# Performance work log

Hardware: AMD Instinct MI355X
Metric: run time of the kernel (lower is better)

The kernel has to match this reference:

```python
import jax, jax.numpy as jnp
import numpy as np

TEMP = 0.07
DIAG_FILL = -10.0


def setup_inputs() -> dict:
    key = jax.random.key(0)
    k1, k2 = jax.random.split(key)
    N, D = 8192, 256
    feat_q = jax.random.normal(k1, (N, D), dtype=jnp.float32)
    feat_k = jax.random.normal(k2, (N, D), dtype=jnp.float32)
    return {"feat_q": feat_q, "feat_k": feat_k}


def reference(feat_q, feat_k):
    # feat_k is detached in the original module
    feat_k = jax.lax.stop_gradient(feat_k)
    N = feat_q.shape[0]

    q_norm = jnp.linalg.norm(feat_q, axis=-1, keepdims=True)  # [N,1]
    k_norm = jnp.linalg.norm(feat_k, axis=-1, keepdims=True)  # [N,1]

    # positive logits: cosine similarity of matching patches -> [N,1]
    l_pos = jnp.sum(feat_q * feat_k, axis=-1, keepdims=True) / (q_norm * k_norm)

    # negative logits: pairwise cosine similarities -> [N,N]
    l_neg = jnp.einsum('nd,md->nm', feat_q, feat_k) / (q_norm * k_norm.T)
    # mask diagonal (self pairs) with -10.0
    diag = jnp.eye(N, dtype=bool)
    l_neg = jnp.where(diag, jnp.float32(DIAG_FILL), l_neg)

    out = jnp.concatenate([l_pos, l_neg], axis=1) / TEMP  # [N, 1+N]
    # cross-entropy with target class 0, reduction='none'
    loss = jax.nn.logsumexp(out, axis=1) - out[:, 0]
    return loss
```

## Files before the change

kernel.cpp:

```cpp
#include <hip/hip_runtime.h>
#include <stdint.h>

#define N_ROWS 8192
#define DIM 256

constexpr float INV_T = 1.0f / 0.07f;
constexpr float M0    = 1.0f / 0.07f;
constexpr float LOG2E = 1.44269504088896f;
constexpr float C1    = INV_T * LOG2E;
constexpr float C0    = -M0 * LOG2E;
constexpr float KSCL  = 127.0f / 0.35f;

typedef int i32x4  __attribute__((ext_vector_type(4)));
typedef int i32x16 __attribute__((ext_vector_type(16)));

__device__ inline float fast_exp2(float x) {
    float r;
    asm("v_exp_f32 %0, %1" : "=v"(r) : "v"(x));
    return r;
}
__device__ inline int pack4(int a, int b, int c, int d) {
    return (a & 0xff) | ((b & 0xff) << 8) | ((c & 0xff) << 16) | (d << 24);
}

__global__ __launch_bounds__(256) void prep_kernel(
    const float* __restrict__ q, const float* __restrict__ k,
    int* __restrict__ qi8, int* __restrict__ ki8,
    float* __restrict__ lposT, float* __restrict__ fqs) {
    const int wid  = threadIdx.x >> 6;
    const int lane = threadIdx.x & 63;
    const int row  = blockIdx.x * 4 + wid;

    const float4 qv = *reinterpret_cast<const float4*>(q + (size_t)row * DIM + lane * 4);
    const float4 kv = *reinterpret_cast<const float4*>(k + (size_t)row * DIM + lane * 4);

    float qq = qv.x*qv.x + qv.y*qv.y + qv.z*qv.z + qv.w*qv.w;
    float kk = kv.x*kv.x + kv.y*kv.y + kv.z*kv.z + kv.w*kv.w;
    float qk = qv.x*kv.x + qv.y*kv.y + qv.z*kv.z + qv.w*kv.w;
    float qm = fmaxf(fmaxf(fabsf(qv.x), fabsf(qv.y)), fmaxf(fabsf(qv.z), fabsf(qv.w)));

    #pragma unroll
    for (int off = 32; off > 0; off >>= 1) {
        qq += __shfl_xor(qq, off, 64);
        kk += __shfl_xor(kk, off, 64);
        qk += __shfl_xor(qk, off, 64);
        qm  = fmaxf(qm, __shfl_xor(qm, off, 64));
    }
    const float iq = 1.0f / sqrtf(qq);
    const float ik = 1.0f / sqrtf(kk);

    const float ksc = ik * KSCL;
    int k0 = __float2int_rn(fminf(fmaxf(kv.x * ksc, -127.f), 127.f));
    int k1 = __float2int_rn(fminf(fmaxf(kv.y * ksc, -127.f), 127.f));
    int k2 = __float2int_rn(fminf(fmaxf(kv.z * ksc, -127.f), 127.f));
    int k3 = __float2int_rn(fminf(fmaxf(kv.w * ksc, -127.f), 127.f));
    ki8[(size_t)row * 64 + lane] = pack4(k0, k1, k2, k3);

    const float qsc = 127.0f / qm;
    int q0 = __float2int_rn(qv.x * qsc);
    int q1 = __float2int_rn(qv.y * qsc);
    int q2 = __float2int_rn(qv.z * qsc);
    int q3 = __float2int_rn(qv.w * qsc);
    qi8[(size_t)row * 64 + lane] = pack4(q0, q1, q2, q3);

    if (lane == 0) {
        lposT[row] = qk * iq * ik * INV_T;
        fqs[row] = C1 * (0.35f / (127.0f * 127.0f)) * qm * iq;
    }
}

__global__ __launch_bounds__(256, 2) void gemm_lse_kernel(
    const uint8_t* __restrict__ qi8, const uint8_t* __restrict__ ki8,
    const float* __restrict__ fqs, float* __restrict__ ps) {
    __shared__ char lds[3 * 16384];

    const int tid  = threadIdx.x;
    const int lane = tid & 63;
    const int wid  = tid >> 6;
    const int l31  = lane & 31;
    const int l5   = lane >> 5;

    const int qtile = blockIdx.x;
    const int strip = blockIdx.y;
    const int qw    = qtile * 256 + wid * 64;
    const int ks0   = strip * 512;

    auto stage = [&](int t) {
        char* dst = lds + (t % 3) * 16384;
        const int kr0 = ks0 + t * 64;
        #pragma unroll
        for (int s = 0; s < 4; ++s) {
            const int n    = wid * 4 + s;
            const int lrow = n * 8 + (lane >> 3);
            const int row  = lrow & 63;
            const int kh   = lrow >> 6;
            const uint8_t* gp = ki8 + (size_t)(kr0 + row) * 256 + kh * 128
                              + (((lane & 7) ^ (lrow & 7)) << 4);
            __builtin_amdgcn_global_load_lds(
                (const __attribute__((address_space(1))) void*)gp,
                (__attribute__((address_space(3))) void*)(dst + n * 1024),
                16, 0, 0);
        }
    };

    i32x4 qf[8][2];
    #pragma unroll
    for (int ks = 0; ks < 8; ++ks)
        #pragma unroll
        for (int cg = 0; cg < 2; ++cg)
            qf[ks][cg] = *reinterpret_cast<const i32x4*>(
                qi8 + (size_t)(qw + cg * 32 + l31) * 256 + ks * 32 + l5 * 16);
    const float f0 = fqs[qw + l31];
    const float f1 = fqs[qw + 32 + l31];

    stage(0);
    stage(1);

    i32x16 acc00 = {}, acc01 = {}, acc10 = {}, acc11 = {};
    float ssum0 = 0.f, ssum1 = 0.f;

    auto lda = [&](const char* src, int rg, i32x4* a) {
        const int row = rg * 32 + l31;
        #pragma unroll
        for (int ks = 0; ks < 8; ++ks) {
            const int o    = ks * 32 + l5 * 16;
            const int lrow = row + ((o >> 7) << 6);
            const int slot = ((o & 127) >> 4) ^ (lrow & 7);
            a[ks] = *reinterpret_cast<const i32x4*>(src + lrow * 128 + (slot << 4));
        }
    };

    auto expfrag = [&](i32x16& A, bool diag, float f, float& ss) {
        float s = 0.f;
        #pragma unroll
        for (int r = 0; r < 16; ++r) {
            float e = fast_exp2(fmaf((float)A[r], f, C0));
            if (diag && (((r & 3) + 8 * (r >> 2) + 4 * l5) == l31)) e = 0.f;
            s += e;
            A[r] = 0;
        }
        ss += s;
    };

    auto epilogue = [&](int t) {
        const int kc0 = ks0 + t * 64;
        expfrag(acc00, kc0 == qw, f0, ssum0);
        expfrag(acc01, false,     f1, ssum1);
        expfrag(acc10, false,     f0, ssum0);
        expfrag(acc11, kc0 == qw, f1, ssum1);
    };

    #pragma unroll
    for (int t = 0; t < 8; ++t) {
        if (t < 7) { asm volatile("s_waitcnt vmcnt(4)" ::: "memory"); }
        else       { asm volatile("s_waitcnt vmcnt(0)" ::: "memory"); }
        __builtin_amdgcn_s_barrier();
        __builtin_amdgcn_sched_barrier(0);
        if (t < 6) stage(t + 2);
        if (t > 0) epilogue(t - 1);

        const char* cur = lds + (t % 3) * 16384;
        i32x4 a0[8], a1[8];
        lda(cur, 0, a0);
        __builtin_amdgcn_s_setprio(1);
        #pragma unroll
        for (int ks = 0; ks < 8; ++ks) {
            acc00 = __builtin_amdgcn_mfma_i32_32x32x32_i8(a0[ks], qf[ks][0], acc00, 0, 0, 0);
            acc01 = __builtin_amdgcn_mfma_i32_32x32x32_i8(a0[ks], qf[ks][1], acc01, 0, 0, 0);
        }
        __builtin_amdgcn_s_setprio(0);
        lda(cur, 1, a1);
        __builtin_amdgcn_s_setprio(1);
        #pragma unroll
        for (int ks = 0; ks < 8; ++ks) {
            acc10 = __builtin_amdgcn_mfma_i32_32x32x32_i8(a1[ks], qf[ks][0], acc10, 0, 0, 0);
            acc11 = __builtin_amdgcn_mfma_i32_32x32x32_i8(a1[ks], qf[ks][1], acc11, 0, 0, 0);
        }
        __builtin_amdgcn_s_setprio(0);
    }
    epilogue(7);

    ssum0 += __shfl_xor(ssum0, 32, 64);
    ssum1 += __shfl_xor(ssum1, 32, 64);
    if (lane < 32) {
        ps[(size_t)(qw + l31) * 16 + strip]      = ssum0;
        ps[(size_t)(qw + 32 + l31) * 16 + strip] = ssum1;
    }
}

__global__ __launch_bounds__(256) void finalize_kernel(
    const float* __restrict__ ps, const float* __restrict__ lposT,
    float* __restrict__ out) {
    const int row = blockIdx.x * 256 + threadIdx.x;
    float S = 0.f;
    #pragma unroll
    for (int c = 0; c < 4; ++c) {
        const float4 p = *reinterpret_cast<const float4*>(ps + (size_t)row * 16 + c * 4);
        S += p.x + p.y + p.z + p.w;
    }
    const float lp = lposT[row];
    S += __expf(lp - M0);
    out[row] = M0 + logf(S) - lp;
}

extern "C" void kernel_launch(void* const* d_in, const int* in_sizes, int n_in,
                              void* d_out, int out_size, void* d_ws, size_t ws_size,
                              hipStream_t stream) {
    const float* q = (const float*)d_in[0];
    const float* k = (const float*)d_in[1];
    float* out = (float*)d_out;

    char* ws = (char*)d_ws;
    int*   qi8 = (int*)(ws);
    int*   ki8 = (int*)(ws + (2u << 20));
    float* lpt = (float*)(ws + (4u << 20));
    float* fqs = (float*)(ws + (4u << 20) + (32u << 10));
    float* ps  = (float*)(ws + (4u << 20) + (64u << 10));

    prep_kernel<<<N_ROWS / 4, 256, 0, stream>>>(q, k, qi8, ki8, lpt, fqs);
    dim3 grid(32, 16);
    gemm_lse_kernel<<<grid, 256, 0, stream>>>((const uint8_t*)qi8, (const uint8_t*)ki8, fqs, ps);
    finalize_kernel<<<N_ROWS / 256, 256, 0, stream>>>(ps, lpt, out);
}
```

Before: 36.91 us.

## Halve K-tile to 32 rows per stage and raise occupancy to 3 blocks

Each pipeline stage in the GEMM+LSE kernel now covers 32 key rows instead of 64, which halves the LDS ring buffer and drops from four to two accumulators per wave. The launch bound rises to 3 blocks per CU, and the main loop runs 16 iterations without unrolling. The aim is to cut register and LDS pressure so more waves can hide latency. The cost is twice as many barriers and waitcnts per strip, and a loop that is no longer unrolled.

```diff
diff --git a/kernel.cpp b/kernel.cpp
--- a/kernel.cpp
+++ b/kernel.cpp
@@ -69,10 +69,10 @@
     }
 }
 
-__global__ __launch_bounds__(256, 2) void gemm_lse_kernel(
+__global__ __launch_bounds__(256, 3) void gemm_lse_kernel(
     const uint8_t* __restrict__ qi8, const uint8_t* __restrict__ ki8,
     const float* __restrict__ fqs, float* __restrict__ ps) {
-    __shared__ char lds[3 * 16384];
+    __shared__ char lds[3 * 8192];
 
     const int tid  = threadIdx.x;
     const int lane = tid & 63;
@@ -86,15 +86,15 @@
     const int ks0   = strip * 512;
 
     auto stage = [&](int t) {
-        char* dst = lds + (t % 3) * 16384;
-        const int kr0 = ks0 + t * 64;
-        #pragma unroll
-        for (int s = 0; s < 4; ++s) {
-            const int n    = wid * 4 + s;
+        char* dst = lds + (t % 3) * 8192;
+        const int kr0 = ks0 + t * 32;
+        #pragma unroll
+        for (int s = 0; s < 2; ++s) {
+            const int n    = wid * 2 + s;
             const int lrow = n * 8 + (lane >> 3);
-            const int row  = lrow & 63;
-            const int kh   = lrow >> 6;
-            const uint8_t* gp = ki8 + (size_t)(kr0 + row) * 256 + kh * 128
+            const int row  = lrow & 31;
+            const int h    = lrow >> 5;
+            const uint8_t* gp = ki8 + (size_t)(kr0 + row) * 256 + h * 128
                               + (((lane & 7) ^ (lrow & 7)) << 4);
             __builtin_amdgcn_global_load_lds(
                 (const __attribute__((address_space(1))) void*)gp,
@@ -116,15 +116,14 @@
     stage(0);
     stage(1);
 
-    i32x16 acc00 = {}, acc01 = {}, acc10 = {}, acc11 = {};
+    i32x16 acc0 = {}, acc1 = {};
     float ssum0 = 0.f, ssum1 = 0.f;
 
-    auto lda = [&](const char* src, int rg, i32x4* a) {
-        const int row = rg * 32 + l31;
+    auto lda = [&](const char* src, i32x4* a) {
         #pragma unroll
         for (int ks = 0; ks < 8; ++ks) {
             const int o    = ks * 32 + l5 * 16;
-            const int lrow = row + ((o >> 7) << 6);
+            const int lrow = l31 + ((o >> 7) << 5);
             const int slot = ((o & 127) >> 4) ^ (lrow & 7);
             a[ks] = *reinterpret_cast<const i32x4*>(src + lrow * 128 + (slot << 4));
         }
@@ -143,42 +142,32 @@
     };
 
     auto epilogue = [&](int t) {
-        const int kc0 = ks0 + t * 64;
-        expfrag(acc00, kc0 == qw, f0, ssum0);
-        expfrag(acc01, false,     f1, ssum1);
-        expfrag(acc10, false,     f0, ssum0);
-        expfrag(acc11, kc0 == qw, f1, ssum1);
-    };
-
-    #pragma unroll
-    for (int t = 0; t < 8; ++t) {
-        if (t < 7) { asm volatile("s_waitcnt vmcnt(4)" ::: "memory"); }
-        else       { asm volatile("s_waitcnt vmcnt(0)" ::: "memory"); }
+        const int kc0 = ks0 + t * 32;
+        expfrag(acc0, kc0 == qw,      f0, ssum0);
+        expfrag(acc1, kc0 == qw + 32, f1, ssum1);
+    };
+
+    #pragma unroll 1
+    for (int t = 0; t < 16; ++t) {
+        if (t < 15) { asm volatile("s_waitcnt vmcnt(2)" ::: "memory"); }
+        else        { asm volatile("s_waitcnt vmcnt(0)" ::: "memory"); }
         __builtin_amdgcn_s_barrier();
         __builtin_amdgcn_sched_barrier(0);
-        if (t < 6) stage(t + 2);
+        if (t < 14) stage(t + 2);
         if (t > 0) epilogue(t - 1);
 
-        const char* cur = lds + (t % 3) * 16384;
-        i32x4 a0[8], a1[8];
-        lda(cur, 0, a0);
+        const char* cur = lds + (t % 3) * 8192;
+        i32x4 a[8];
+        lda(cur, a);
         __builtin_amdgcn_s_setprio(1);
         #pragma unroll
         for (int ks = 0; ks < 8; ++ks) {
-            acc00 = __builtin_amdgcn_mfma_i32_32x32x32_i8(a0[ks], qf[ks][0], acc00, 0, 0, 0);
-            acc01 = __builtin_amdgcn_mfma_i32_32x32x32_i8(a0[ks], qf[ks][1], acc01, 0, 0, 0);
+            acc0 = __builtin_amdgcn_mfma_i32_32x32x32_i8(a[ks], qf[ks][0], acc0, 0, 0, 0);
+            acc1 = __builtin_amdgcn_mfma_i32_32x32x32_i8(a[ks], qf[ks][1], acc1, 0, 0, 0);
         }
         __builtin_amdgcn_s_setprio(0);
-        lda(cur, 1, a1);
-        __builtin_amdgcn_s_setprio(1);
-        #pragma unroll
-        for (int ks = 0; ks < 8; ++ks) {
-            acc10 = __builtin_amdgcn_mfma_i32_32x32x32_i8(a1[ks], qf[ks][0], acc10, 0, 0, 0);
-            acc11 = __builtin_amdgcn_mfma_i32_32x32x32_i8(a1[ks], qf[ks][1], acc11, 0, 0, 0);
-        }
-        __builtin_amdgcn_s_setprio(0);
-    }
-    epilogue(7);
+    }
+    epilogue(15);
 
     ssum0 += __shfl_xor(ssum0, 32, 64);
     ssum1 += __shfl_xor(ssum1, 32, 64);
```

After: 38.44 us. 4.1% more time.

## Interleave exp epilogue of each accumulator pair between MFMA halves

Applied to the files above, without the earlier changes.

Splits the exp/sum epilogue so the acc00/acc01 fragments are processed right after their MFMAs finish (while acc10/acc11 MFMAs run next), and the acc10/acc11 fragments are deferred to the next iteration before the first-half MFMAs. It also splits the inner exp loop into four independent partial sums to shorten dependency chains, and drops the second setprio raise. The aim is to overlap transcendental VALU work with matrix-core execution rather than running it in one block. The risk is extra register pressure and the compiler possibly serialising VALU reads of accumulators against in-flight MFMAs.

```diff
diff --git a/kernel.cpp b/kernel.cpp
--- a/kernel.cpp
+++ b/kernel.cpp
@@ -131,23 +131,24 @@
     };
 
     auto expfrag = [&](i32x16& A, bool diag, float f, float& ss) {
-        float s = 0.f;
-        #pragma unroll
-        for (int r = 0; r < 16; ++r) {
-            float e = fast_exp2(fmaf((float)A[r], f, C0));
-            if (diag && (((r & 3) + 8 * (r >> 2) + 4 * l5) == l31)) e = 0.f;
-            s += e;
-            A[r] = 0;
-        }
-        ss += s;
-    };
-
-    auto epilogue = [&](int t) {
-        const int kc0 = ks0 + t * 64;
-        expfrag(acc00, kc0 == qw, f0, ssum0);
-        expfrag(acc01, false,     f1, ssum1);
-        expfrag(acc10, false,     f0, ssum0);
-        expfrag(acc11, kc0 == qw, f1, ssum1);
+        float s0 = 0.f, s1 = 0.f, s2 = 0.f, s3 = 0.f;
+        #pragma unroll
+        for (int r = 0; r < 16; r += 4) {
+            float e0 = fast_exp2(fmaf((float)A[r],     f, C0));
+            float e1 = fast_exp2(fmaf((float)A[r + 1], f, C0));
+            float e2 = fast_exp2(fmaf((float)A[r + 2], f, C0));
+            float e3 = fast_exp2(fmaf((float)A[r + 3], f, C0));
+            if (diag) {
+                const int base = 8 * (r >> 2) + 4 * l5;
+                if (base + 0 == l31) e0 = 0.f;
+                if (base + 1 == l31) e1 = 0.f;
+                if (base + 2 == l31) e2 = 0.f;
+                if (base + 3 == l31) e3 = 0.f;
+            }
+            s0 += e0; s1 += e1; s2 += e2; s3 += e3;
+            A[r] = 0; A[r + 1] = 0; A[r + 2] = 0; A[r + 3] = 0;
+        }
+        ss += (s0 + s1) + (s2 + s3);
     };
 
     #pragma unroll
@@ -157,11 +158,17 @@
         __builtin_amdgcn_s_barrier();
         __builtin_amdgcn_sched_barrier(0);
         if (t < 6) stage(t + 2);
-        if (t > 0) epilogue(t - 1);
 
         const char* cur = lds + (t % 3) * 16384;
         i32x4 a0[8], a1[8];
         lda(cur, 0, a0);
+
+        if (t > 0) {
+            const int kp = ks0 + (t - 1) * 64;
+            expfrag(acc10, false,    f0, ssum0);
+            expfrag(acc11, kp == qw, f1, ssum1);
+        }
+
         __builtin_amdgcn_s_setprio(1);
         #pragma unroll
         for (int ks = 0; ks < 8; ++ks) {
@@ -169,16 +176,26 @@
             acc01 = __builtin_amdgcn_mfma_i32_32x32x32_i8(a0[ks], qf[ks][1], acc01, 0, 0, 0);
         }
         __builtin_amdgcn_s_setprio(0);
+
         lda(cur, 1, a1);
-        __builtin_amdgcn_s_setprio(1);
+
+        {
+            const int kc0 = ks0 + t * 64;
+            expfrag(acc00, kc0 == qw, f0, ssum0);
+            expfrag(acc01, false,     f1, ssum1);
+        }
+
         #pragma unroll
         for (int ks = 0; ks < 8; ++ks) {
             acc10 = __builtin_amdgcn_mfma_i32_32x32x32_i8(a1[ks], qf[ks][0], acc10, 0, 0, 0);
             acc11 = __builtin_amdgcn_mfma_i32_32x32x32_i8(a1[ks], qf[ks][1], acc11, 0, 0, 0);
         }
-        __builtin_amdgcn_s_setprio(0);
-    }
-    epilogue(7);
+    }
+    {
+        const int kp = ks0 + 7 * 64;
+        expfrag(acc10, false,    f0, ssum0);
+        expfrag(acc11, kp == qw, f1, ssum1);
+    }
 
     ssum0 += __shfl_xor(ssum0, 32, 64);
     ssum1 += __shfl_xor(ssum1, 32, 64);
```

New measurement: 134.2 us. 3.63x slower.
